# Kernel tuning notes

Hardware: AMD Instinct MI355X
Metric: run time of the kernel (lower is better)

Reference implementation:

```python
import math
import jax, jax.numpy as jnp
import numpy as np

B, T, C = 2, 2048, 1024
HEADS = 16
HD = C // HEADS  # 64


def setup_inputs() -> dict:
    key = jax.random.key(0)
    ks = jax.random.split(key, 5)
    s = 0.02
    return {
        "x": jax.random.normal(ks[0], (B, T, C), jnp.float32),
        "Wq": jax.random.normal(ks[1], (C, C), jnp.float32) * s,
        "bq": jnp.zeros((C,), jnp.float32),
        "Wk": jax.random.normal(ks[2], (C, HD), jnp.float32) * s,
        "bk": jnp.zeros((HD,), jnp.float32),
        "Wv": jax.random.normal(ks[3], (C, HD), jnp.float32) * s,
        "bv": jnp.zeros((HD,), jnp.float32),
        "Wo": jax.random.normal(ks[4], (C, C), jnp.float32) * s,
        "bo": jnp.zeros((C,), jnp.float32),
    }


def _rope_tables(seq_len, dim):
    pos = jnp.arange(seq_len, dtype=jnp.float32)
    freqs = 1.0 / (10000.0 ** (jnp.arange(0, dim, 2, dtype=jnp.float32) / dim))
    ang = pos[:, None] * freqs[None, :]          # (T, dim//2)
    # broadcast over (B, T, H, dim//2)
    return jnp.sin(ang)[None, :, None, :], jnp.cos(ang)[None, :, None, :]


def _apply_rope(t, sin, cos, dim):
    t1, t2 = t[..., : dim // 2], t[..., dim // 2 :]
    # matches torch source: emb[..., :d/2]=sin, emb[..., d/2:]=cos
    return jnp.concatenate([t1 * cos + t2 * sin, t1 * sin - t2 * cos], axis=-1)


def reference(x, Wq, bq, Wk, bk, Wv, bv, Wo, bo):
    Bx, Tx, Cx = x.shape
    q = (x @ Wq + bq).reshape(Bx, Tx, HEADS, HD)   # (B,T,H,hd)
    k = (x @ Wk + bk)[:, :, None, :]               # (B,T,1,hd) single KV head (MQA)
    v = (x @ Wv + bv)[:, :, None, :]
    sin, cos = _rope_tables(Tx, HD)
    q = _apply_rope(q, sin, cos, HD)
    k = _apply_rope(k, sin, cos, HD)
    att = jnp.einsum('bthd,bThd->bhtT', q, k) / math.sqrt(HD)
    causal = jnp.triu(jnp.ones((Tx, Tx), bool), 1)
    att = jnp.where(causal, -jnp.inf, att)
    att = jax.nn.softmax(att, axis=-1)
    out = jnp.einsum('bhtT,bThd->bthd', att, v).reshape(Bx, Tx, Cx)
    return out @ Wo + bo
```

## Files before the change

### kernel.cpp

```cpp
#include <hip/hip_runtime.h>
#include <math.h>

#define BSZ   2
#define TSEQ  2048
#define CDIM  1024
#define NHEAD 16
#define HDIM  64
#define BT    (BSZ*TSEQ)
#define NQKV  1152

typedef __attribute__((ext_vector_type(8))) short short8;
typedef __attribute__((ext_vector_type(4))) float f32x4;
typedef unsigned short u16;
typedef unsigned int   u32;

__device__ __forceinline__ u16 f2b(float f) {
    union { float f; u32 u; } c; c.f = f;
    u32 u = c.u;
    u += 0x7fffu + ((u >> 16) & 1u);
    return (u16)(u >> 16);
}
__device__ __forceinline__ u32 pack2(float lo, float hi) {
    return (u32)f2b(lo) | ((u32)f2b(hi) << 16);
}

__device__ __forceinline__ void async_copy16(const void* g, void* l) {
    __builtin_amdgcn_global_load_lds(
        (__attribute__((address_space(1))) const void*)g,
        (__attribute__((address_space(3))) void*)l,
        16, 0, 0);
}

__device__ __forceinline__ void transpose_tile(
    const float* __restrict__ W, u16* __restrict__ Wt,
    int K, int Nw, int nofs, int bx, int by, float (*T)[65])
{
    const int tid = threadIdx.x;
    const int k0 = by * 64, n0 = bx * 64;
    #pragma unroll
    for (int i = 0; i < 16; ++i) {
        int idx = i * 256 + tid, r = idx >> 6, c = idx & 63;
        T[r][c] = W[(size_t)(k0 + r) * Nw + n0 + c];
    }
    __syncthreads();
    #pragma unroll
    for (int i = 0; i < 16; ++i) {
        int idx = i * 256 + tid, rn = idx >> 6, ck = idx & 63;
        Wt[(size_t)(nofs + n0 + rn) * K + k0 + ck] = f2b(T[ck][rn]);
    }
}

__global__ __launch_bounds__(256) void prep_kernel(
    const float* __restrict__ x,
    const float* __restrict__ Wq, const float* __restrict__ Wk,
    const float* __restrict__ Wv, const float* __restrict__ Wo,
    const float* __restrict__ bq, const float* __restrict__ bk,
    const float* __restrict__ bv,
    u16* __restrict__ xb,
    u16* __restrict__ Wqkvt, u16* __restrict__ Wot, float* __restrict__ bqkv)
{
    __shared__ float T[64][65];
    const int bid = blockIdx.x;
    if (bid < 4096) {
        int i = bid * 256 + threadIdx.x;
        float4 f = ((const float4*)x)[i];
        u16* d = xb + (size_t)i * 4;
        d[0] = f2b(f.x); d[1] = f2b(f.y); d[2] = f2b(f.z); d[3] = f2b(f.w);
    } else if (bid < 4352) {
        int b2 = bid - 4096;
        transpose_tile(Wq, Wqkvt, 1024, 1024, 0, b2 & 15, b2 >> 4, T);
    } else if (bid < 4368) {
        transpose_tile(Wk, Wqkvt, 1024, 64, 1024, 0, bid - 4352, T);
    } else if (bid < 4384) {
        transpose_tile(Wv, Wqkvt, 1024, 64, 1088, 0, bid - 4368, T);
    } else if (bid < 4640) {
        int b2 = bid - 4384;
        transpose_tile(Wo, Wot, 1024, 1024, 0, b2 & 15, b2 >> 4, T);
    } else {
        for (int i = threadIdx.x; i < NQKV; i += 256)
            bqkv[i] = (i < 1024) ? bq[i] : (i < 1088 ? bk[i - 1024] : bv[i - 1088]);
    }
}

__global__ __launch_bounds__(256) void gemm_qkv_kernel(
    const u16* __restrict__ A, const u16* __restrict__ Bt,
    const float* __restrict__ bias,
    u16* __restrict__ qb, u16* __restrict__ kb, u16* __restrict__ vT)
{
    __shared__ __align__(16) u16 AsC[64 * 32];
    __shared__ __align__(16) u16 BsC[128 * 32];
    const int tid  = threadIdx.x;
    const int wave = tid >> 6, lane = tid & 63;
    const int ln16 = lane & 15, quad = lane >> 4;
    const int wm = wave >> 1, wn = wave & 1;
    const int m0 = blockIdx.y * 64, n0 = blockIdx.x * 128;
    const int K = CDIM;

    const int c_row = ((tid >> 6) << 4) + (tid & 15);
    const int c_k   = ((tid >> 4) & 3) * 8;
    const u16* ag  = &A [(size_t)(m0 + c_row)       * K + c_k];
    const u16* bg0 = &Bt[(size_t)(n0 + c_row)       * K + c_k];
    const u16* bg1 = &Bt[(size_t)(n0 + 64 + c_row)  * K + c_k];
    u16* a_l  = &AsC[(size_t)wave * 64 * 8];
    u16* b_l0 = &BsC[(size_t)wave * 64 * 8];
    u16* b_l1 = &BsC[(size_t)(wave + 4) * 64 * 8];

    f32x4 acc[2][4];
    #pragma unroll
    for (int i = 0; i < 2; ++i)
        #pragma unroll
        for (int j = 0; j < 4; ++j) acc[i][j] = (f32x4){0.f, 0.f, 0.f, 0.f};

    for (int k0 = 0; k0 < K; k0 += 32) {
        async_copy16(ag,  a_l);
        async_copy16(bg0, b_l0);
        async_copy16(bg1, b_l1);
        ag += 32; bg0 += 32; bg1 += 32;
        __syncthreads();

        short8 af[2], bf[4];
        #pragma unroll
        for (int mt = 0; mt < 2; ++mt)
            af[mt] = *(const short8*)&AsC[(((wm * 2 + mt) * 64) + quad * 16 + ln16) * 8];
        #pragma unroll
        for (int nt = 0; nt < 4; ++nt)
            bf[nt] = *(const short8*)&BsC[(((wn * 4 + nt) * 64) + quad * 16 + ln16) * 8];
        #pragma unroll
        for (int mt = 0; mt < 2; ++mt)
            #pragma unroll
            for (int nt = 0; nt < 4; ++nt)
                acc[mt][nt] = __builtin_amdgcn_mfma_f32_16x16x32_bf16(
                    af[mt], bf[nt], acc[mt][nt], 0, 0, 0);
        __syncthreads();
    }

    #pragma unroll
    for (int mt = 0; mt < 2; ++mt)
        #pragma unroll
        for (int nt = 0; nt < 4; ++nt) {
            float bb = bias[n0 + wn * 64 + nt * 16 + ln16];
            #pragma unroll
            for (int r = 0; r < 4; ++r) acc[mt][nt][r] += bb;
        }

    const int col0 = n0 + wn * 64;
    if (col0 < 1024) {
        const int hh = col0 >> 6;
        #pragma unroll
        for (int nt = 0; nt < 2; ++nt) {
            int j = nt * 16 + ln16;
            float fr = exp2f(-0.41524101186092029f * (float)j);
            #pragma unroll
            for (int mt = 0; mt < 2; ++mt)
                #pragma unroll
                for (int r = 0; r < 4; ++r) {
                    int m = m0 + wm * 32 + mt * 16 + quad * 4 + r;
                    float sn, cs;
                    __sincosf((float)(m & (TSEQ - 1)) * fr, &sn, &cs);
                    float t1 = acc[mt][nt][r], t2 = acc[mt][nt + 2][r];
                    u16* o = qb + (size_t)m * CDIM + hh * 64 + j;
                    o[0]  = f2b(fmaf(t1, cs,  t2 * sn) * 0.18033688011112043f);
                    o[32] = f2b(fmaf(t1, sn, -t2 * cs) * 0.18033688011112043f);
                }
        }
    } else if (wn == 0) {
        #pragma unroll
        for (int nt = 0; nt < 2; ++nt) {
            int j = nt * 16 + ln16;
            float fr = exp2f(-0.41524101186092029f * (float)j);
            #pragma unroll
            for (int mt = 0; mt < 2; ++mt)
                #pragma unroll
                for (int r = 0; r < 4; ++r) {
                    int m = m0 + wm * 32 + mt * 16 + quad * 4 + r;
                    float sn, cs;
                    __sincosf((float)(m & (TSEQ - 1)) * fr, &sn, &cs);
                    float t1 = acc[mt][nt][r], t2 = acc[mt][nt + 2][r];
                    u16* o = kb + (size_t)m * HDIM + j;
                    o[0]  = f2b(fmaf(t1, cs,  t2 * sn));
                    o[32] = f2b(fmaf(t1, sn, -t2 * cs));
                }
        }
    } else {
        #pragma unroll
        for (int nt = 0; nt < 4; ++nt) {
            int d = nt * 16 + ln16;
            #pragma unroll
            for (int mt = 0; mt < 2; ++mt) {
                int mr = m0 + wm * 32 + mt * 16 + quad * 4;
                int b  = mr >> 11, tq = mr & (TSEQ - 1);
                uint2 val;
                val.x = pack2(acc[mt][nt][0], acc[mt][nt][1]);
                val.y = pack2(acc[mt][nt][2], acc[mt][nt][3]);
                *(uint2*)&vT[(size_t)(b * HDIM + d) * TSEQ + tq] = val;
            }
        }
    }
}

__global__ __launch_bounds__(256) void gemm_mfma_kernel(
    const u16* __restrict__ A, const u16* __restrict__ Bt,
    const float* __restrict__ bias, float* __restrict__ Y,
    int M, int N, int K)
{
    __shared__ __align__(16) u16 AsC[64 * 32];
    __shared__ __align__(16) u16 BsC[128 * 32];
    const int tid  = threadIdx.x;
    const int wave = tid >> 6, lane = tid & 63;
    const int ln16 = lane & 15, quad = lane >> 4;
    const int wm = wave >> 1, wn = wave & 1;
    const int m0 = blockIdx.y * 64, n0 = blockIdx.x * 128;

    const int c_row = ((tid >> 6) << 4) + (tid & 15);
    const int c_k   = ((tid >> 4) & 3) * 8;
    const u16* ag  = &A [(size_t)(m0 + c_row)       * K + c_k];
    const u16* bg0 = &Bt[(size_t)(n0 + c_row)       * K + c_k];
    const u16* bg1 = &Bt[(size_t)(n0 + 64 + c_row)  * K + c_k];
    u16* a_l  = &AsC[(size_t)wave * 64 * 8];
    u16* b_l0 = &BsC[(size_t)wave * 64 * 8];
    u16* b_l1 = &BsC[(size_t)(wave + 4) * 64 * 8];

    f32x4 acc[2][4];
    #pragma unroll
    for (int i = 0; i < 2; ++i)
        #pragma unroll
        for (int j = 0; j < 4; ++j) acc[i][j] = (f32x4){0.f, 0.f, 0.f, 0.f};

    for (int k0 = 0; k0 < K; k0 += 32) {
        async_copy16(ag,  a_l);
        async_copy16(bg0, b_l0);
        async_copy16(bg1, b_l1);
        ag += 32; bg0 += 32; bg1 += 32;
        __syncthreads();

        short8 af[2], bf[4];
        #pragma unroll
        for (int mt = 0; mt < 2; ++mt)
            af[mt] = *(const short8*)&AsC[(((wm * 2 + mt) * 64) + quad * 16 + ln16) * 8];
        #pragma unroll
        for (int nt = 0; nt < 4; ++nt)
            bf[nt] = *(const short8*)&BsC[(((wn * 4 + nt) * 64) + quad * 16 + ln16) * 8];
        #pragma unroll
        for (int mt = 0; mt < 2; ++mt)
            #pragma unroll
            for (int nt = 0; nt < 4; ++nt)
                acc[mt][nt] = __builtin_amdgcn_mfma_f32_16x16x32_bf16(
                    af[mt], bf[nt], acc[mt][nt], 0, 0, 0);
        __syncthreads();
    }

    #pragma unroll
    for (int mt = 0; mt < 2; ++mt)
        #pragma unroll
        for (int nt = 0; nt < 4; ++nt) {
            int n = n0 + wn * 64 + nt * 16 + ln16;
            float bb = bias[n];
            #pragma unroll
            for (int r = 0; r < 4; ++r) {
                int m = m0 + wm * 32 + mt * 16 + quad * 4 + r;
                Y[(size_t)m * N + n] = acc[mt][nt][r] + bb;
            }
        }
}

__device__ __forceinline__ void flash_stage_kv(
    const u16* __restrict__ kb, const u16* __restrict__ vT,
    int b, int kt, u16* __restrict__ Ksb, u16* __restrict__ Vsb,
    const int* row_c, const int* off_c, int c0)
{
    const size_t kt0 = (size_t)(b * TSEQ + kt * 64);
    #pragma unroll
    for (int hf = 0; hf < 2; ++hf) {
        int cc = c0 + hf * 256;
        async_copy16(kb + (kt0 + row_c[hf]) * HDIM + off_c[hf], Ksb + cc * 8);
        async_copy16(vT + (size_t)(b * HDIM + row_c[hf]) * TSEQ + kt * 64 + off_c[hf],
                     Vsb + cc * 8);
    }
}

__device__ __forceinline__ void flash_tile(
    const u16* __restrict__ Ksb, const u16* __restrict__ Vsb,
    const u16* __restrict__ Qs, u16* __restrict__ Pw,
    int wave, int ln16, int quad, bool diag,
    float* lsum, f32x4* oacc)
{
    f32x4 sv[4];
    #pragma unroll
    for (int t = 0; t < 4; ++t) sv[t] = (f32x4){0.f, 0.f, 0.f, 0.f};
    #pragma unroll
    for (int kk2 = 0; kk2 < 2; ++kk2) {
        short8 af = *(const short8*)&Qs[(wave * 128 + kk2 * 64 + quad * 16 + ln16) * 8];
        #pragma unroll
        for (int t = 0; t < 4; ++t) {
            short8 bf = *(const short8*)&Ksb[(t * 128 + kk2 * 64 + quad * 16 + ln16) * 8];
            sv[t] = __builtin_amdgcn_mfma_f32_16x16x32_bf16(af, bf, sv[t], 0, 0, 0);
        }
    }

    if (diag) {
        #pragma unroll
        for (int t = 0; t < 4; ++t) {
            int key = t * 16 + ln16;
            #pragma unroll
            for (int r = 0; r < 4; ++r) {
                float e = (key > wave * 16 + quad * 4 + r) ? 0.f : exp2f(sv[t][r]);
                u32 bits = __float_as_uint(e);
                lsum[r] += __uint_as_float(bits & 0xffff0000u);
                Pw[(quad * 4 + r) * 72 + t * 16 + ln16] = (u16)(bits >> 16);
            }
        }
    } else {
        #pragma unroll
        for (int t = 0; t < 4; ++t)
            #pragma unroll
            for (int r = 0; r < 4; ++r) {
                float e = exp2f(sv[t][r]);
                u32 bits = __float_as_uint(e);
                lsum[r] += __uint_as_float(bits & 0xffff0000u);
                Pw[(quad * 4 + r) * 72 + t * 16 + ln16] = (u16)(bits >> 16);
            }
    }

    #pragma unroll
    for (int kk2 = 0; kk2 < 2; ++kk2) {
        short8 pf = *(const short8*)&Pw[ln16 * 72 + kk2 * 32 + quad * 8];
        #pragma unroll
        for (int t = 0; t < 4; ++t) {
            short8 vf = *(const short8*)&Vsb[(t * 128 + kk2 * 64 + quad * 16 + ln16) * 8];
            oacc[t] = __builtin_amdgcn_mfma_f32_16x16x32_bf16(pf, vf, oacc[t], 0, 0, 0);
        }
    }
}

__global__ __launch_bounds__(256) void flash_mfma_kernel(
    const u16* __restrict__ qb, const u16* __restrict__ kb,
    const u16* __restrict__ vT, u16* __restrict__ o)
{
    const int id  = blockIdx.x;
    const int qt  = 31 - (id >> 5);
    const int hb  = id & 31;
    const int h   = hb >> 1;
    const int b   = hb & 1;
    __shared__ __align__(16) u16 Qs [512 * 8];
    __shared__ __align__(16) u16 Ks0[512 * 8];
    __shared__ __align__(16) u16 Ks1[512 * 8];
    __shared__ __align__(16) u16 Vs0[512 * 8];
    __shared__ __align__(16) u16 Vs1[512 * 8];
    __shared__ __align__(16) u16 Ps[4 * 16 * 72];

    const int tid  = threadIdx.x;
    const int wave = tid >> 6, lane = tid & 63;
    const int ln16 = lane & 15, quad = lane >> 4;

    const int c0 = tid;
    int row_c[2], off_c[2];
    #pragma unroll
    for (int hf = 0; hf < 2; ++hf) {
        int c = c0 + hf * 256;
        row_c[hf] = ((c >> 7) << 4) | (c & 15);
        off_c[hf] = ((c >> 6) & 1) * 32 + ((c >> 4) & 3) * 8;
    }

    u16* Pw = &Ps[wave * 16 * 72];

    #pragma unroll
    for (int hf = 0; hf < 2; ++hf)
        async_copy16(
            qb + (size_t)(b * TSEQ + qt * 64 + row_c[hf]) * CDIM + h * HDIM + off_c[hf],
            Qs + (c0 + hf * 256) * 8);
    flash_stage_kv(kb, vT, b, 0, Ks0, Vs0, row_c, off_c, c0);

    float lsum[4];
    f32x4 oacc[4];
    #pragma unroll
    for (int r = 0; r < 4; ++r) lsum[r] = 0.f;
    #pragma unroll
    for (int t = 0; t < 4; ++t) oacc[t] = (f32x4){0.f, 0.f, 0.f, 0.f};

    int kt = 0;
    while (true) {
        __syncthreads();
        if (kt < qt) flash_stage_kv(kb, vT, b, kt + 1, Ks1, Vs1, row_c, off_c, c0);
        flash_tile(Ks0, Vs0, Qs, Pw, wave, ln16, quad, kt == qt, lsum, oacc);
        if (++kt > qt) break;
        __syncthreads();
        if (kt < qt) flash_stage_kv(kb, vT, b, kt + 1, Ks0, Vs0, row_c, off_c, c0);
        flash_tile(Ks1, Vs1, Qs, Pw, wave, ln16, quad, kt == qt, lsum, oacc);
        if (++kt > qt) break;
    }

    float inv[4];
    #pragma unroll
    for (int r = 0; r < 4; ++r) {
        float l = lsum[r];
        #pragma unroll
        for (int off = 1; off < 16; off <<= 1)
            l += __shfl_xor(l, off, 64);
        inv[r] = 1.0f / l;
    }
    #pragma unroll
    for (int t = 0; t < 4; ++t) {
        #pragma unroll
        for (int r = 0; r < 4; ++r) {
            int row = qt * 64 + wave * 16 + quad * 4 + r;
            int d   = t * 16 + ln16;
            o[(size_t)(b * TSEQ + row) * CDIM + h * HDIM + d] = f2b(oacc[t][r] * inv[r]);
        }
    }
}

extern "C" void kernel_launch(void* const* d_in, const int* in_sizes, int n_in,
                              void* d_out, int out_size, void* d_ws, size_t ws_size,
                              hipStream_t stream)
{
    const float* x  = (const float*)d_in[0];
    const float* Wq = (const float*)d_in[1];
    const float* bq = (const float*)d_in[2];
    const float* Wk = (const float*)d_in[3];
    const float* bk = (const float*)d_in[4];
    const float* Wv = (const float*)d_in[5];
    const float* bv = (const float*)d_in[6];
    const float* Wo = (const float*)d_in[7];
    const float* bo = (const float*)d_in[8];
    float* out = (float*)d_out;

    const size_t MB = 1u << 20;
    char* w = (char*)d_ws;
    u16*   xb   = (u16*)(w);
    u16*   aob  = (u16*)(w);
    u16*   qb   = (u16*)(w + 8 * MB);
    u16*   kb   = (u16*)(w + 16 * MB);
    u16*   vT   = (u16*)(w + 16 * MB + 512 * 1024);
    u16*   Wqkvt= (u16*)(w + 17 * MB);
    u16*   Wot  = (u16*)(w + 20 * MB);
    float* bqkv = (float*)(w + 22 * MB);

    prep_kernel<<<dim3(4641), dim3(256), 0, stream>>>(
        x, Wq, Wk, Wv, Wo, bq, bk, bv, xb, Wqkvt, Wot, bqkv);
    gemm_qkv_kernel<<<dim3(NQKV / 128, BT / 64), dim3(256), 0, stream>>>(
        xb, Wqkvt, bqkv, qb, kb, vT);
    flash_mfma_kernel<<<dim3(32 * NHEAD * BSZ), dim3(256), 0, stream>>>(
        qb, kb, vT, aob);
    gemm_mfma_kernel<<<dim3(CDIM / 128, BT / 64), dim3(256), 0, stream>>>(
        aob, Wot, bo, out, BT, CDIM, CDIM);
}
```

Baseline: 192.4 us.

## Pair complementary causal query tiles per flash block to share K/V loads

Each flash-attention block now handles two query tiles, p and 31-p, so every block does the same amount of causal work, and K/V tiles staged in shared memory are reused by both query tiles. The grid is halved to 512 blocks and K/V fragments are held in registers across the two MFMA passes. This removes load imbalance across blocks from causal masking and halves K/V global traffic, at the cost of more registers and LDS per block, which may lower occupancy, and fewer blocks to fill the 256 CUs.

```diff
diff --git a/kernel.cpp b/kernel.cpp
--- a/kernel.cpp
+++ b/kernel.cpp
@@ -263,40 +263,10 @@
         }
 }
 
-__device__ __forceinline__ void flash_stage_kv(
-    const u16* __restrict__ kb, const u16* __restrict__ vT,
-    int b, int kt, u16* __restrict__ Ksb, u16* __restrict__ Vsb,
-    const int* row_c, const int* off_c, int c0)
-{
-    const size_t kt0 = (size_t)(b * TSEQ + kt * 64);
-    #pragma unroll
-    for (int hf = 0; hf < 2; ++hf) {
-        int cc = c0 + hf * 256;
-        async_copy16(kb + (kt0 + row_c[hf]) * HDIM + off_c[hf], Ksb + cc * 8);
-        async_copy16(vT + (size_t)(b * HDIM + row_c[hf]) * TSEQ + kt * 64 + off_c[hf],
-                     Vsb + cc * 8);
-    }
-}
-
-__device__ __forceinline__ void flash_tile(
-    const u16* __restrict__ Ksb, const u16* __restrict__ Vsb,
-    const u16* __restrict__ Qs, u16* __restrict__ Pw,
-    int wave, int ln16, int quad, bool diag,
-    float* lsum, f32x4* oacc)
-{
-    f32x4 sv[4];
-    #pragma unroll
-    for (int t = 0; t < 4; ++t) sv[t] = (f32x4){0.f, 0.f, 0.f, 0.f};
-    #pragma unroll
-    for (int kk2 = 0; kk2 < 2; ++kk2) {
-        short8 af = *(const short8*)&Qs[(wave * 128 + kk2 * 64 + quad * 16 + ln16) * 8];
-        #pragma unroll
-        for (int t = 0; t < 4; ++t) {
-            short8 bf = *(const short8*)&Ksb[(t * 128 + kk2 * 64 + quad * 16 + ln16) * 8];
-            sv[t] = __builtin_amdgcn_mfma_f32_16x16x32_bf16(af, bf, sv[t], 0, 0, 0);
-        }
-    }
-
+__device__ __forceinline__ void flash_softmax_store(
+    f32x4* sv, u16* __restrict__ Pw, int wave, int ln16, int quad,
+    bool diag, float* lsum)
+{
     if (diag) {
         #pragma unroll
         for (int t = 0; t < 4; ++t) {
@@ -320,14 +290,68 @@
                 Pw[(quad * 4 + r) * 72 + t * 16 + ln16] = (u16)(bits >> 16);
             }
     }
-
+}
+
+__device__ __forceinline__ void flash_tile_pair(
+    const u16* __restrict__ Ksb, const u16* __restrict__ Vsb,
+    const u16* __restrict__ Qsa, const u16* __restrict__ Qsb,
+    u16* __restrict__ Pwa, u16* __restrict__ Pwb,
+    int wave, int ln16, int quad,
+    bool do_a, bool diag_a, bool diag_b,
+    float* lsa, float* lsb, f32x4* oa, f32x4* ob)
+{
+    short8 kf[2][4];
+    #pragma unroll
+    for (int kk2 = 0; kk2 < 2; ++kk2)
+        #pragma unroll
+        for (int t = 0; t < 4; ++t)
+            kf[kk2][t] = *(const short8*)&Ksb[(t * 128 + kk2 * 64 + quad * 16 + ln16) * 8];
+
+    f32x4 svb[4], sva[4];
+    #pragma unroll
+    for (int t = 0; t < 4; ++t) svb[t] = (f32x4){0.f, 0.f, 0.f, 0.f};
     #pragma unroll
     for (int kk2 = 0; kk2 < 2; ++kk2) {
-        short8 pf = *(const short8*)&Pw[ln16 * 72 + kk2 * 32 + quad * 8];
-        #pragma unroll
-        for (int t = 0; t < 4; ++t) {
-            short8 vf = *(const short8*)&Vsb[(t * 128 + kk2 * 64 + quad * 16 + ln16) * 8];
-            oacc[t] = __builtin_amdgcn_mfma_f32_16x16x32_bf16(pf, vf, oacc[t], 0, 0, 0);
+        short8 qf = *(const short8*)&Qsb[(wave * 128 + kk2 * 64 + quad * 16 + ln16) * 8];
+        #pragma unroll
+        for (int t = 0; t < 4; ++t)
+            svb[t] = __builtin_amdgcn_mfma_f32_16x16x32_bf16(qf, kf[kk2][t], svb[t], 0, 0, 0);
+    }
+    if (do_a) {
+        #pragma unroll
+        for (int t = 0; t < 4; ++t) sva[t] = (f32x4){0.f, 0.f, 0.f, 0.f};
+        #pragma unroll
+        for (int kk2 = 0; kk2 < 2; ++kk2) {
+            short8 qf = *(const short8*)&Qsa[(wave * 128 + kk2 * 64 + quad * 16 + ln16) * 8];
+            #pragma unroll
+            for (int t = 0; t < 4; ++t)
+                sva[t] = __builtin_amdgcn_mfma_f32_16x16x32_bf16(qf, kf[kk2][t], sva[t], 0, 0, 0);
+        }
+    }
+
+    flash_softmax_store(svb, Pwb, wave, ln16, quad, diag_b, lsb);
+    if (do_a) flash_softmax_store(sva, Pwa, wave, ln16, quad, diag_a, lsa);
+
+    short8 vf[2][4];
+    #pragma unroll
+    for (int kk2 = 0; kk2 < 2; ++kk2)
+        #pragma unroll
+        for (int t = 0; t < 4; ++t)
+            vf[kk2][t] = *(const short8*)&Vsb[(t * 128 + kk2 * 64 + quad * 16 + ln16) * 8];
+    #pragma unroll
+    for (int kk2 = 0; kk2 < 2; ++kk2) {
+        short8 pf = *(const short8*)&Pwb[ln16 * 72 + kk2 * 32 + quad * 8];
+        #pragma unroll
+        for (int t = 0; t < 4; ++t)
+            ob[t] = __builtin_amdgcn_mfma_f32_16x16x32_bf16(pf, vf[kk2][t], ob[t], 0, 0, 0);
+    }
+    if (do_a) {
+        #pragma unroll
+        for (int kk2 = 0; kk2 < 2; ++kk2) {
+            short8 pf = *(const short8*)&Pwa[ln16 * 72 + kk2 * 32 + quad * 8];
+            #pragma unroll
+            for (int t = 0; t < 4; ++t)
+                oa[t] = __builtin_amdgcn_mfma_f32_16x16x32_bf16(pf, vf[kk2][t], oa[t], 0, 0, 0);
         }
     }
 }
@@ -337,16 +361,16 @@
     const u16* __restrict__ vT, u16* __restrict__ o)
 {
     const int id  = blockIdx.x;
-    const int qt  = 31 - (id >> 5);
+    const int p   = id >> 5;
     const int hb  = id & 31;
     const int h   = hb >> 1;
     const int b   = hb & 1;
-    __shared__ __align__(16) u16 Qs [512 * 8];
-    __shared__ __align__(16) u16 Ks0[512 * 8];
-    __shared__ __align__(16) u16 Ks1[512 * 8];
-    __shared__ __align__(16) u16 Vs0[512 * 8];
-    __shared__ __align__(16) u16 Vs1[512 * 8];
-    __shared__ __align__(16) u16 Ps[4 * 16 * 72];
+    const int qta = p, qtb = 31 - p;
+
+    __shared__ __align__(16) u16 Qsa[512 * 8], Qsb[512 * 8];
+    __shared__ __align__(16) u16 Ks0[512 * 8], Ks1[512 * 8];
+    __shared__ __align__(16) u16 Vs0[512 * 8], Vs1[512 * 8];
+    __shared__ __align__(16) u16 Psa[4 * 16 * 72], Psb[4 * 16 * 72];
 
     const int tid  = threadIdx.x;
     const int wave = tid >> 6, lane = tid & 63;
@@ -361,50 +385,86 @@
         off_c[hf] = ((c >> 6) & 1) * 32 + ((c >> 4) & 3) * 8;
     }
 
-    u16* Pw = &Ps[wave * 16 * 72];
-
-    #pragma unroll
-    for (int hf = 0; hf < 2; ++hf)
-        async_copy16(
-            qb + (size_t)(b * TSEQ + qt * 64 + row_c[hf]) * CDIM + h * HDIM + off_c[hf],
-            Qs + (c0 + hf * 256) * 8);
-    flash_stage_kv(kb, vT, b, 0, Ks0, Vs0, row_c, off_c, c0);
-
-    float lsum[4];
-    f32x4 oacc[4];
-    #pragma unroll
-    for (int r = 0; r < 4; ++r) lsum[r] = 0.f;
-    #pragma unroll
-    for (int t = 0; t < 4; ++t) oacc[t] = (f32x4){0.f, 0.f, 0.f, 0.f};
+    const u16* kg[2]; const u16* vg[2];
+    #pragma unroll
+    for (int hf = 0; hf < 2; ++hf) {
+        kg[hf] = kb + (size_t)(b * TSEQ + row_c[hf]) * HDIM + off_c[hf];
+        vg[hf] = vT + (size_t)(b * HDIM + row_c[hf]) * TSEQ + off_c[hf];
+    }
+
+    u16* Pwa = &Psa[wave * 16 * 72];
+    u16* Pwb = &Psb[wave * 16 * 72];
+
+    #pragma unroll
+    for (int hf = 0; hf < 2; ++hf) {
+        size_t qoff = (size_t)(b * TSEQ + row_c[hf]) * CDIM + h * HDIM + off_c[hf];
+        async_copy16(qb + qoff + (size_t)qta * 64 * CDIM, Qsa + (c0 + hf * 256) * 8);
+        async_copy16(qb + qoff + (size_t)qtb * 64 * CDIM, Qsb + (c0 + hf * 256) * 8);
+        int cc = c0 + hf * 256;
+        async_copy16(kg[hf], Ks0 + cc * 8);
+        async_copy16(vg[hf], Vs0 + cc * 8);
+    }
+
+    float lsa[4], lsb[4];
+    f32x4 oa[4], ob[4];
+    #pragma unroll
+    for (int r = 0; r < 4; ++r) { lsa[r] = 0.f; lsb[r] = 0.f; }
+    #pragma unroll
+    for (int t = 0; t < 4; ++t) {
+        oa[t] = (f32x4){0.f, 0.f, 0.f, 0.f};
+        ob[t] = (f32x4){0.f, 0.f, 0.f, 0.f};
+    }
 
     int kt = 0;
     while (true) {
         __syncthreads();
-        if (kt < qt) flash_stage_kv(kb, vT, b, kt + 1, Ks1, Vs1, row_c, off_c, c0);
-        flash_tile(Ks0, Vs0, Qs, Pw, wave, ln16, quad, kt == qt, lsum, oacc);
-        if (++kt > qt) break;
+        if (kt < qtb) {
+            #pragma unroll
+            for (int hf = 0; hf < 2; ++hf) {
+                int cc = c0 + hf * 256;
+                async_copy16(kg[hf] + (size_t)(kt + 1) * 64 * HDIM, Ks1 + cc * 8);
+                async_copy16(vg[hf] + (size_t)(kt + 1) * 64,        Vs1 + cc * 8);
+            }
+        }
+        flash_tile_pair(Ks0, Vs0, Qsa, Qsb, Pwa, Pwb, wave, ln16, quad,
+                        kt <= qta, kt == qta, kt == qtb, lsa, lsb, oa, ob);
+        if (++kt > qtb) break;
         __syncthreads();
-        if (kt < qt) flash_stage_kv(kb, vT, b, kt + 1, Ks0, Vs0, row_c, off_c, c0);
-        flash_tile(Ks1, Vs1, Qs, Pw, wave, ln16, quad, kt == qt, lsum, oacc);
-        if (++kt > qt) break;
-    }
-
-    float inv[4];
-    #pragma unroll
-    for (int r = 0; r < 4; ++r) {
-        float l = lsum[r];
-        #pragma unroll
-        for (int off = 1; off < 16; off <<= 1)
-            l += __shfl_xor(l, off, 64);
-        inv[r] = 1.0f / l;
-    }
-    #pragma unroll
-    for (int t = 0; t < 4; ++t) {
+        if (kt < qtb) {
+            #pragma unroll
+            for (int hf = 0; hf < 2; ++hf) {
+                int cc = c0 + hf * 256;
+                async_copy16(kg[hf] + (size_t)(kt + 1) * 64 * HDIM, Ks0 + cc * 8);
+                async_copy16(vg[hf] + (size_t)(kt + 1) * 64,        Vs0 + cc * 8);
+            }
+        }
+        flash_tile_pair(Ks1, Vs1, Qsa, Qsb, Pwa, Pwb, wave, ln16, quad,
+                        kt <= qta, kt == qta, kt == qtb, lsa, lsb, oa, ob);
+        if (++kt > qtb) break;
+    }
+
+    #pragma unroll
+    for (int s = 0; s < 2; ++s) {
+        float* ls   = s ? lsb : lsa;
+        f32x4* oacc = s ? ob  : oa;
+        int    qt   = s ? qtb : qta;
+        float inv[4];
         #pragma unroll
         for (int r = 0; r < 4; ++r) {
-            int row = qt * 64 + wave * 16 + quad * 4 + r;
-            int d   = t * 16 + ln16;
-            o[(size_t)(b * TSEQ + row) * CDIM + h * HDIM + d] = f2b(oacc[t][r] * inv[r]);
+            float l = ls[r];
+            #pragma unroll
+            for (int off = 1; off < 16; off <<= 1)
+                l += __shfl_xor(l, off, 64);
+            inv[r] = 1.0f / l;
+        }
+        #pragma unroll
+        for (int t = 0; t < 4; ++t) {
+            #pragma unroll
+            for (int r = 0; r < 4; ++r) {
+                int row = qt * 64 + wave * 16 + quad * 4 + r;
+                int d   = t * 16 + ln16;
+                o[(size_t)(b * TSEQ + row) * CDIM + h * HDIM + d] = f2b(oacc[t][r] * inv[r]);
+            }
         }
     }
 }
@@ -439,7 +499,7 @@
         x, Wq, Wk, Wv, Wo, bq, bk, bv, xb, Wqkvt, Wot, bqkv);
     gemm_qkv_kernel<<<dim3(NQKV / 128, BT / 64), dim3(256), 0, stream>>>(
         xb, Wqkvt, bqkv, qb, kb, vT);
-    flash_mfma_kernel<<<dim3(32 * NHEAD * BSZ), dim3(256), 0, stream>>>(
+    flash_mfma_kernel<<<dim3(16 * NHEAD * BSZ), dim3(256), 0, stream>>>(
         qb, kb, vT, aob);
     gemm_mfma_kernel<<<dim3(CDIM / 128, BT / 64), dim3(256), 0, stream>>>(
         aob, Wot, bo, out, BT, CDIM, CDIM);
```

Result: slower. 198.7 us (+3.3%).

## Double flash-attention query tile to 128 rows per block for K/V reuse

Applied to the files above, without the earlier changes.

Each flash-attention block now covers 128 query rows instead of 64, with each wave owning two 16-row m-tiles. Every staged K/V tile therefore feeds twice as many MFMAs, halving K/V traffic and per-tile barrier overhead. Waves skip tiles that lie entirely above their causal boundary and mask only partial tiles. In exchange, the grid shrinks to 512 blocks, per-thread register use and LDS grow, and waves within a block become more imbalanced near the diagonal.

```diff
diff --git a/kernel.cpp b/kernel.cpp
--- a/kernel.cpp
+++ b/kernel.cpp
@@ -281,54 +281,78 @@
 __device__ __forceinline__ void flash_tile(
     const u16* __restrict__ Ksb, const u16* __restrict__ Vsb,
     const u16* __restrict__ Qs, u16* __restrict__ Pw,
-    int wave, int ln16, int quad, bool diag,
-    float* lsum, f32x4* oacc)
-{
-    f32x4 sv[4];
-    #pragma unroll
-    for (int t = 0; t < 4; ++t) sv[t] = (f32x4){0.f, 0.f, 0.f, 0.f};
+    int wave, int ln16, int quad, int Rw, int kt,
+    float (*lsum)[4], f32x4 (*oacc)[4])
+{
+    if (kt * 64 > Rw + 31) return;
+
+    f32x4 sv[2][4];
+    #pragma unroll
+    for (int mt = 0; mt < 2; ++mt)
+        #pragma unroll
+        for (int t = 0; t < 4; ++t) sv[mt][t] = (f32x4){0.f, 0.f, 0.f, 0.f};
     #pragma unroll
     for (int kk2 = 0; kk2 < 2; ++kk2) {
-        short8 af = *(const short8*)&Qs[(wave * 128 + kk2 * 64 + quad * 16 + ln16) * 8];
-        #pragma unroll
-        for (int t = 0; t < 4; ++t) {
-            short8 bf = *(const short8*)&Ksb[(t * 128 + kk2 * 64 + quad * 16 + ln16) * 8];
-            sv[t] = __builtin_amdgcn_mfma_f32_16x16x32_bf16(af, bf, sv[t], 0, 0, 0);
-        }
-    }
-
-    if (diag) {
-        #pragma unroll
-        for (int t = 0; t < 4; ++t) {
-            int key = t * 16 + ln16;
-            #pragma unroll
-            for (int r = 0; r < 4; ++r) {
-                float e = (key > wave * 16 + quad * 4 + r) ? 0.f : exp2f(sv[t][r]);
-                u32 bits = __float_as_uint(e);
-                lsum[r] += __uint_as_float(bits & 0xffff0000u);
-                Pw[(quad * 4 + r) * 72 + t * 16 + ln16] = (u16)(bits >> 16);
+        short8 af[2], bf[4];
+        #pragma unroll
+        for (int mt = 0; mt < 2; ++mt)
+            af[mt] = *(const short8*)&Qs[((wave * 2 + mt) * 128 + (kk2 * 4 + quad) * 16 + ln16) * 8];
+        #pragma unroll
+        for (int t = 0; t < 4; ++t)
+            bf[t] = *(const short8*)&Ksb[(t * 128 + kk2 * 64 + quad * 16 + ln16) * 8];
+        #pragma unroll
+        for (int mt = 0; mt < 2; ++mt)
+            #pragma unroll
+            for (int t = 0; t < 4; ++t)
+                sv[mt][t] = __builtin_amdgcn_mfma_f32_16x16x32_bf16(
+                    af[mt], bf[t], sv[mt][t], 0, 0, 0);
+    }
+
+    const bool full = (kt * 64 + 63 <= Rw);
+    const int thr = Rw - kt * 64 + quad * 4;
+    if (full) {
+        #pragma unroll
+        for (int mt = 0; mt < 2; ++mt)
+            #pragma unroll
+            for (int t = 0; t < 4; ++t)
+                #pragma unroll
+                for (int r = 0; r < 4; ++r) {
+                    float e = exp2f(sv[mt][t][r]);
+                    u32 bits = __float_as_uint(e);
+                    lsum[mt][r] += __uint_as_float(bits & 0xffff0000u);
+                    Pw[(mt * 16 + quad * 4 + r) * 72 + t * 16 + ln16] = (u16)(bits >> 16);
+                }
+    } else {
+        #pragma unroll
+        for (int mt = 0; mt < 2; ++mt)
+            #pragma unroll
+            for (int t = 0; t < 4; ++t) {
+                int key = t * 16 + ln16;
+                #pragma unroll
+                for (int r = 0; r < 4; ++r) {
+                    float e = (key > thr + mt * 16 + r) ? 0.f : exp2f(sv[mt][t][r]);
+                    u32 bits = __float_as_uint(e);
+                    lsum[mt][r] += __uint_as_float(bits & 0xffff0000u);
+                    Pw[(mt * 16 + quad * 4 + r) * 72 + t * 16 + ln16] = (u16)(bits >> 16);
+                }
             }
-        }
-    } else {
-        #pragma unroll
-        for (int t = 0; t < 4; ++t)
-            #pragma unroll
-            for (int r = 0; r < 4; ++r) {
-                float e = exp2f(sv[t][r]);
-                u32 bits = __float_as_uint(e);
-                lsum[r] += __uint_as_float(bits & 0xffff0000u);
-                Pw[(quad * 4 + r) * 72 + t * 16 + ln16] = (u16)(bits >> 16);
-            }
     }
 
     #pragma unroll
     for (int kk2 = 0; kk2 < 2; ++kk2) {
-        short8 pf = *(const short8*)&Pw[ln16 * 72 + kk2 * 32 + quad * 8];
-        #pragma unroll
-        for (int t = 0; t < 4; ++t) {
-            short8 vf = *(const short8*)&Vsb[(t * 128 + kk2 * 64 + quad * 16 + ln16) * 8];
-            oacc[t] = __builtin_amdgcn_mfma_f32_16x16x32_bf16(pf, vf, oacc[t], 0, 0, 0);
-        }
+        short8 pf[2], vf[4];
+        #pragma unroll
+        for (int mt = 0; mt < 2; ++mt)
+            pf[mt] = *(const short8*)&Pw[(mt * 16 + ln16) * 72 + kk2 * 32 + quad * 8];
+        #pragma unroll
+        for (int nt = 0; nt < 4; ++nt)
+            vf[nt] = *(const short8*)&Vsb[(nt * 128 + kk2 * 64 + quad * 16 + ln16) * 8];
+        #pragma unroll
+        for (int mt = 0; mt < 2; ++mt)
+            #pragma unroll
+            for (int nt = 0; nt < 4; ++nt)
+                oacc[mt][nt] = __builtin_amdgcn_mfma_f32_16x16x32_bf16(
+                    pf[mt], vf[nt], oacc[mt][nt], 0, 0, 0);
     }
 }
 
@@ -337,20 +361,23 @@
     const u16* __restrict__ vT, u16* __restrict__ o)
 {
     const int id  = blockIdx.x;
-    const int qt  = 31 - (id >> 5);
+    const int p   = 15 - (id >> 5);
     const int hb  = id & 31;
     const int h   = hb >> 1;
     const int b   = hb & 1;
-    __shared__ __align__(16) u16 Qs [512 * 8];
+    const int ktmax = 2 * p + 1;
+
+    __shared__ __align__(16) u16 Qs [1024 * 8];
     __shared__ __align__(16) u16 Ks0[512 * 8];
     __shared__ __align__(16) u16 Ks1[512 * 8];
     __shared__ __align__(16) u16 Vs0[512 * 8];
     __shared__ __align__(16) u16 Vs1[512 * 8];
-    __shared__ __align__(16) u16 Ps[4 * 16 * 72];
+    __shared__ __align__(16) u16 Ps[4 * 32 * 72];
 
     const int tid  = threadIdx.x;
     const int wave = tid >> 6, lane = tid & 63;
     const int ln16 = lane & 15, quad = lane >> 4;
+    const int Rw   = p * 128 + wave * 32;
 
     const int c0 = tid;
     int row_c[2], off_c[2];
@@ -361,50 +388,61 @@
         off_c[hf] = ((c >> 6) & 1) * 32 + ((c >> 4) & 3) * 8;
     }
 
-    u16* Pw = &Ps[wave * 16 * 72];
-
-    #pragma unroll
-    for (int hf = 0; hf < 2; ++hf)
+    u16* Pw = &Ps[wave * 32 * 72];
+
+    #pragma unroll
+    for (int i = 0; i < 4; ++i) {
+        int c = tid + i * 256;
+        int rt = c >> 7, koff8 = (c >> 4) & 7, ln = c & 15;
         async_copy16(
-            qb + (size_t)(b * TSEQ + qt * 64 + row_c[hf]) * CDIM + h * HDIM + off_c[hf],
-            Qs + (c0 + hf * 256) * 8);
+            qb + (size_t)(b * TSEQ + p * 128 + rt * 16 + ln) * CDIM + h * HDIM + koff8 * 8,
+            Qs + c * 8);
+    }
     flash_stage_kv(kb, vT, b, 0, Ks0, Vs0, row_c, off_c, c0);
 
-    float lsum[4];
-    f32x4 oacc[4];
-    #pragma unroll
-    for (int r = 0; r < 4; ++r) lsum[r] = 0.f;
-    #pragma unroll
-    for (int t = 0; t < 4; ++t) oacc[t] = (f32x4){0.f, 0.f, 0.f, 0.f};
+    float lsum[2][4];
+    f32x4 oacc[2][4];
+    #pragma unroll
+    for (int mt = 0; mt < 2; ++mt)
+        #pragma unroll
+        for (int r = 0; r < 4; ++r) lsum[mt][r] = 0.f;
+    #pragma unroll
+    for (int mt = 0; mt < 2; ++mt)
+        #pragma unroll
+        for (int nt = 0; nt < 4; ++nt) oacc[mt][nt] = (f32x4){0.f, 0.f, 0.f, 0.f};
 
     int kt = 0;
     while (true) {
         __syncthreads();
-        if (kt < qt) flash_stage_kv(kb, vT, b, kt + 1, Ks1, Vs1, row_c, off_c, c0);
-        flash_tile(Ks0, Vs0, Qs, Pw, wave, ln16, quad, kt == qt, lsum, oacc);
-        if (++kt > qt) break;
-        __syncthreads();
-        if (kt < qt) flash_stage_kv(kb, vT, b, kt + 1, Ks0, Vs0, row_c, off_c, c0);
-        flash_tile(Ks1, Vs1, Qs, Pw, wave, ln16, quad, kt == qt, lsum, oacc);
-        if (++kt > qt) break;
-    }
-
-    float inv[4];
-    #pragma unroll
-    for (int r = 0; r < 4; ++r) {
-        float l = lsum[r];
-        #pragma unroll
-        for (int off = 1; off < 16; off <<= 1)
-            l += __shfl_xor(l, off, 64);
-        inv[r] = 1.0f / l;
-    }
-    #pragma unroll
-    for (int t = 0; t < 4; ++t) {
+        if (kt < ktmax) flash_stage_kv(kb, vT, b, kt + 1, Ks1, Vs1, row_c, off_c, c0);
+        flash_tile(Ks0, Vs0, Qs, Pw, wave, ln16, quad, Rw, kt, lsum, oacc);
+        if (++kt > ktmax) break;
+        __syncthreads();
+        if (kt < ktmax) flash_stage_kv(kb, vT, b, kt + 1, Ks0, Vs0, row_c, off_c, c0);
+        flash_tile(Ks1, Vs1, Qs, Pw, wave, ln16, quad, Rw, kt, lsum, oacc);
+        if (++kt > ktmax) break;
+    }
+
+    #pragma unroll
+    for (int mt = 0; mt < 2; ++mt) {
+        float inv[4];
         #pragma unroll
         for (int r = 0; r < 4; ++r) {
-            int row = qt * 64 + wave * 16 + quad * 4 + r;
-            int d   = t * 16 + ln16;
-            o[(size_t)(b * TSEQ + row) * CDIM + h * HDIM + d] = f2b(oacc[t][r] * inv[r]);
+            float l = lsum[mt][r];
+            #pragma unroll
+            for (int off = 1; off < 16; off <<= 1)
+                l += __shfl_xor(l, off, 64);
+            inv[r] = 1.0f / l;
+        }
+        #pragma unroll
+        for (int nt = 0; nt < 4; ++nt) {
+            #pragma unroll
+            for (int r = 0; r < 4; ++r) {
+                int row = Rw + mt * 16 + quad * 4 + r;
+                int d   = nt * 16 + ln16;
+                o[(size_t)(b * TSEQ + row) * CDIM + h * HDIM + d] =
+                    f2b(oacc[mt][nt][r] * inv[r]);
+            }
         }
     }
 }
@@ -439,7 +477,7 @@
         x, Wq, Wk, Wv, Wo, bq, bk, bv, xb, Wqkvt, Wot, bqkv);
     gemm_qkv_kernel<<<dim3(NQKV / 128, BT / 64), dim3(256), 0, stream>>>(
         xb, Wqkvt, bqkv, qb, kb, vT);
-    flash_mfma_kernel<<<dim3(32 * NHEAD * BSZ), dim3(256), 0, stream>>>(
+    flash_mfma_kernel<<<dim3(16 * NHEAD * BSZ), dim3(256), 0, stream>>>(
         qb, kb, vT, aob);
     gemm_mfma_kernel<<<dim3(CDIM / 128, BT / 64), dim3(256), 0, stream>>>(
         aob, Wot, bo, out, BT, CDIM, CDIM);
```

After: 203.0 us. +5.5%, slower.
